# Kernel tuning notes

Measured on AMD Instinct MI355X. Metric: run time of the kernel, lower is better.

The kernel has to match this reference:

```python
import jax, jax.numpy as jnp
import numpy as np
import math

DIM_IN = 512
DIM_OUT = 512
KERNEL = 3
STYLE_DIM = 2 * 128
LIN_SCALE = 1.0 / math.sqrt(STYLE_DIM)      # EqualLinear scale (lr_mul=1)
CONV_SCALE = 1.0 / math.sqrt(DIM_IN * KERNEL ** 2)  # fan_in = dim_in * k**2 (as in source)
PAD = KERNEL // 2


def setup_inputs() -> dict:
    key = jax.random.key(0)
    ks = jax.random.split(key, 5)
    B, T = 16, 2048
    x = jax.random.normal(ks[0], (B, DIM_IN, T), dtype=jnp.float32)
    c_src = jax.random.normal(ks[1], (B, 128), dtype=jnp.float32)
    c_trg = jax.random.normal(ks[2], (B, 128), dtype=jnp.float32)
    style_w = jax.random.normal(ks[3], (DIM_IN, STYLE_DIM), dtype=jnp.float32)
    style_b = jnp.ones((DIM_IN,), dtype=jnp.float32)  # bias_init=1
    weight = jax.random.normal(ks[4], (1, DIM_OUT, DIM_IN, KERNEL), dtype=jnp.float32)
    return {"x": x, "c_src": c_src, "c_trg": c_trg,
            "style_w": style_w, "style_b": style_b, "weight": weight}


def reference(x, c_src, c_trg, style_w, style_b, weight):
    B = x.shape[0]
    # EqualLinear: style code s [B, dim_in]
    c = jnp.concatenate([c_src, c_trg], axis=-1)              # [B, 256]
    s = c @ (style_w * LIN_SCALE).T + style_b                 # [B, dim_in]
    # Modulate: w [B, dim_out, dim_in, k]
    w = CONV_SCALE * weight * s[:, None, :, None]
    # Demodulate over (dim_in, k)
    demod = jax.lax.rsqrt(jnp.sum(w * w, axis=(2, 3)) + 1e-8)  # [B, dim_out]
    w = w * demod[:, :, None, None]
    # Per-sample conv1d, padding 'same' (pad = k//2), vmapped over batch
    def conv1(xi, wi):
        # xi: [dim_in, T], wi: [dim_out, dim_in, k]
        out = jax.lax.conv_general_dilated(
            xi[None], wi, window_strides=(1,), padding=[(PAD, PAD)],
            dimension_numbers=("NCH", "OIH", "NCH"))
        return out[0]                                          # [dim_out, T]
    return jax.vmap(conv1)(x, w)                               # [B, dim_out, T]
```

## Files before the change

### kernel.cpp

```cpp
#include <hip/hip_runtime.h>
#include <cstdint>
#include <cstddef>


#define LIN_SCALE  0.0625f
#define CONV_SCALE 0.014731391f

#define B_   16
#define CIN  512
#define COUT 512
#define T_   2048
#define TP   2050

typedef __bf16 bf16x8 __attribute__((ext_vector_type(8)));
typedef float  f32x4  __attribute__((ext_vector_type(4)));
typedef unsigned short u16x8 __attribute__((ext_vector_type(8)));
typedef unsigned short u16x2 __attribute__((ext_vector_type(2)));

#define AS1 __attribute__((address_space(1)))
#define AS3 __attribute__((address_space(3)))

__device__ inline unsigned short f2bf(float f) {
  __bf16 h = (__bf16)f;
  return __builtin_bit_cast(unsigned short, h);
}

__global__ __launch_bounds__(256) void style_kernel(const float* __restrict__ c_src,
                                                    const float* __restrict__ c_trg,
                                                    const float* __restrict__ sw,
                                                    const float* __restrict__ sb,
                                                    float* __restrict__ s) {
  __shared__ float c[256];
  const int b = blockIdx.y;
  const int tid = threadIdx.x;
  c[tid] = (tid < 128) ? c_src[b * 128 + tid] : c_trg[b * 128 + tid - 128];
  __syncthreads();
  const int w = tid >> 6, lane = tid & 63;
  #pragma unroll
  for (int rr = 0; rr < 16; ++rr) {
    const int i = blockIdx.x * 64 + w * 16 + rr;
    const float* row = sw + (size_t)i * 256;
    float acc = row[lane] * c[lane] + row[lane + 64] * c[lane + 64]
              + row[lane + 128] * c[lane + 128] + row[lane + 192] * c[lane + 192];
    #pragma unroll
    for (int off = 32; off; off >>= 1) acc += __shfl_down(acc, off, 64);
    if (lane == 0) s[b * 512 + i] = acc * LIN_SCALE + sb[i];
  }
}

__global__ __launch_bounds__(256) void modw_kernel(const float* __restrict__ weight,
                                                   const float* __restrict__ s,
                                                   unsigned short* __restrict__ Wm) {
  const int o = blockIdx.x;
  const int tid = threadIdx.x;
  __shared__ float wsh[1536];
  __shared__ float svs[16 * 512];
  __shared__ float partial[16][4];
  __shared__ float demv[16];

  #pragma unroll
  for (int j = tid; j < 1536; j += 256) wsh[j] = weight[(size_t)o * 1536 + j];
  #pragma unroll
  for (int j = tid; j < 16 * 512; j += 256) svs[j] = s[j];
  __syncthreads();

  float wr[6];
  #pragma unroll
  for (int q = 0; q < 6; ++q) wr[q] = wsh[tid * 6 + q] * CONV_SCALE;

  const int lane = tid & 63, w = tid >> 6;
  float ssb[16];
  #pragma unroll
  for (int b = 0; b < 16; ++b) {
    const float s0 = svs[b * 512 + 2 * tid];
    const float s1 = svs[b * 512 + 2 * tid + 1];
    float ss = 0.f;
    #pragma unroll
    for (int q = 0; q < 3; ++q) { float v = wr[q] * s0; ss += v * v; }
    #pragma unroll
    for (int q = 3; q < 6; ++q) { float v = wr[q] * s1; ss += v * v; }
    ssb[b] = ss;
  }
  #pragma unroll
  for (int b = 0; b < 16; ++b) {
    float ss = ssb[b];
    #pragma unroll
    for (int off = 32; off; off >>= 1) ss += __shfl_down(ss, off, 64);
    if (lane == 0) partial[b][w] = ss;
  }
  __syncthreads();
  if (tid < 16)
    demv[tid] = rsqrtf(partial[tid][0] + partial[tid][1] + partial[tid][2] + partial[tid][3] + 1e-8f);
  __syncthreads();

  #pragma unroll
  for (int b = 0; b < 16; ++b) {
    const float dem = demv[b];
    const float s0 = svs[b * 512 + 2 * tid] * dem;
    const float s1 = svs[b * 512 + 2 * tid + 1] * dem;
    #pragma unroll
    for (int k = 0; k < 3; ++k) {
      u16x2 v;
      v.x = f2bf(wr[k] * s0);
      v.y = f2bf(wr[3 + k] * s1);
      *(u16x2*)&Wm[(((size_t)b * 3 + k) * 512 + o) * 512 + 2 * tid] = v;
    }
  }
}

__global__ __launch_bounds__(256) void transpose_kernel(const float* __restrict__ x,
                                                        unsigned short* __restrict__ xT) {
  __shared__ float tile[64][65];
  const int b = blockIdx.z, i0 = blockIdx.y * 64, t0 = blockIdx.x * 64;
  const int tid = threadIdx.x;

  const int lr = tid >> 4;
  const int lc = (tid & 15) * 4;
  const float* xb = x + ((size_t)b * CIN + i0) * T_ + t0;
  #pragma unroll
  for (int p = 0; p < 4; ++p) {
    const int r = p * 16 + lr;
    const float4 v = *(const float4*)(xb + (size_t)r * T_ + lc);
    tile[r][lc + 0] = v.x; tile[r][lc + 1] = v.y;
    tile[r][lc + 2] = v.z; tile[r][lc + 3] = v.w;
  }
  if (blockIdx.x == 0 && tid < 8)
    *(u16x8*)&xT[(size_t)b * TP * CIN + i0 + tid * 8] = (u16x8){0,0,0,0,0,0,0,0};
  if (blockIdx.x == gridDim.x - 1 && tid < 8)
    *(u16x8*)&xT[((size_t)b * TP + TP - 1) * CIN + i0 + tid * 8] = (u16x8){0,0,0,0,0,0,0,0};
  __syncthreads();

  const int st = tid >> 3;
  const int si = (tid & 7) * 8;
  unsigned short* xTb = xT + ((size_t)b * TP + 1 + t0) * CIN + i0;
  #pragma unroll
  for (int p = 0; p < 2; ++p) {
    const int t = p * 32 + st;
    u16x8 v;
    #pragma unroll
    for (int q = 0; q < 8; ++q) v[q] = f2bf(tile[si + q][t]);
    *(u16x8*)&xTb[(size_t)t * CIN + si] = v;
  }
}

#define BM 128
#define BN 256
#define BK 32

__global__ __launch_bounds__(256, 2) void gemm_kernel(const unsigned short* __restrict__ Wm,
                                                      const unsigned short* __restrict__ xT,
                                                      float* __restrict__ out) {
  __shared__ unsigned short lA[3 * 128 * 32];
  __shared__ unsigned short lB[258 * 32];

  const int id  = blockIdx.x;
  const int xcd = id & 7;
  const int j   = id >> 3;
  const int b   = xcd + 8 * (j >> 5);
  const int r   = j & 31;
  const int o0  = (r >> 3) * BM;
  const int t0  = (r & 7) * BN;

  const int tid  = threadIdx.x;
  const int lane = tid & 63;
  const int wm   = ((tid >> 6) & 1) * 64;
  const int wn   = (tid >> 7) * 128;
  const int rl   = lane & 15;
  const int kc   = lane >> 4;

  const unsigned short* gW = Wm + ((size_t)b * 3 * 512 + o0) * 512;
  const unsigned short* gX = xT + ((size_t)b * TP + t0) * CIN;

  f32x4 acc[4][8];
  #pragma unroll
  for (int i = 0; i < 4; ++i)
    #pragma unroll
    for (int jj = 0; jj < 8; ++jj) acc[i][jj] = (f32x4){0.f, 0.f, 0.f, 0.f};

  for (int kk = 0; kk < 16; ++kk) {
    const int i0 = kk * 32;
    __syncthreads();
    #pragma unroll
    for (int q = 0; q < 6; ++q) {
      const int ci  = q * 256 + tid;
      const int row = ci >> 2;
      const int tap = row >> 7;
      const int ar  = row & 127;
      const int gc  = ((ci & 3) ^ ((ar >> 1) & 3)) * 8;
      __builtin_amdgcn_global_load_lds(
          (const AS1 void*)(gW + (size_t)tap * 262144 + (size_t)ar * 512 + i0 + gc),
          (AS3 void*)(&lA[ci * 8]), 16, 0, 0);
    }
    #pragma unroll
    for (int q = 0; q < 4; ++q) {
      const int ci  = q * 256 + tid;
      const int row = ci >> 2;
      const int gc  = ((ci & 3) ^ ((row >> 1) & 3)) * 8;
      __builtin_amdgcn_global_load_lds(
          (const AS1 void*)(gX + (size_t)row * CIN + i0 + gc),
          (AS3 void*)(&lB[ci * 8]), 16, 0, 0);
    }
    if (tid < 8) {
      const int ci  = 1024 + tid;
      const int row = ci >> 2;
      const int gc  = ((ci & 3) ^ ((row >> 1) & 3)) * 8;
      __builtin_amdgcn_global_load_lds(
          (const AS1 void*)(gX + (size_t)row * CIN + i0 + gc),
          (AS3 void*)(&lB[ci * 8]), 16, 0, 0);
    }
    __syncthreads();

    #pragma unroll
    for (int tap = 0; tap < 3; ++tap) {
      bf16x8 af[4], bfr[8];
      #pragma unroll
      for (int mi = 0; mi < 4; ++mi) {
        const int ra = wm + mi * 16 + rl;
        af[mi] = *(const bf16x8*)&lA[((tap * 128 + ra) * 4 + (kc ^ ((ra >> 1) & 3))) * 8];
      }
      #pragma unroll
      for (int ni = 0; ni < 8; ++ni) {
        const int rb = wn + ni * 16 + rl + tap;
        bfr[ni] = *(const bf16x8*)&lB[(rb * 4 + (kc ^ ((rb >> 1) & 3))) * 8];
      }
      #pragma unroll
      for (int mi = 0; mi < 4; ++mi)
        #pragma unroll
        for (int ni = 0; ni < 8; ++ni)
          acc[mi][ni] = __builtin_amdgcn_mfma_f32_16x16x32_bf16(af[mi], bfr[ni], acc[mi][ni], 0, 0, 0);
    }
  }

  float* ob = out + ((size_t)b * COUT + o0 + wm) * T_ + t0 + wn;
  const int rrow = (lane >> 4) * 4;
  const int ccol = lane & 15;
  #pragma unroll
  for (int mi = 0; mi < 4; ++mi)
    #pragma unroll
    for (int ni = 0; ni < 8; ++ni)
      #pragma unroll
      for (int rr = 0; rr < 4; ++rr)
        ob[(size_t)(mi * 16 + rrow + rr) * T_ + ni * 16 + ccol] = acc[mi][ni][rr];
}

extern "C" void kernel_launch(void* const* d_in, const int* in_sizes, int n_in,
                              void* d_out, int out_size, void* d_ws, size_t ws_size,
                              hipStream_t stream) {
  const float* x       = (const float*)d_in[0];
  const float* c_src   = (const float*)d_in[1];
  const float* c_trg   = (const float*)d_in[2];
  const float* style_w = (const float*)d_in[3];
  const float* style_b = (const float*)d_in[4];
  const float* weight  = (const float*)d_in[5];
  float* out = (float*)d_out;

  char* ws = (char*)d_ws;
  float* s_buf          = (float*)ws;
  unsigned short* Wm    = (unsigned short*)(ws + 32768);
  unsigned short* xTbuf = (unsigned short*)(ws + 32768 + 25165824);

  style_kernel<<<dim3(8, 16), 256, 0, stream>>>(c_src, c_trg, style_w, style_b, s_buf);
  modw_kernel<<<dim3(COUT), 256, 0, stream>>>(weight, s_buf, Wm);
  transpose_kernel<<<dim3(T_ / 64, CIN / 64, B_), 256, 0, stream>>>(x, xTbuf);
  gemm_kernel<<<dim3(512), 256, 0, stream>>>(Wm, xTbuf, out);
}
```

Baseline: 187.1 us.

## Warp-specialize GEMM with a producer wave double-buffering LDS tiles

Adds a fifth wavefront to each GEMM block that issues every global-to-LDS tile load into a double buffer. The four compute waves now synchronize through LDS ready/done counters instead of block-wide barriers. The aim is to overlap memory loads with MFMA work and to take the load issue off the compute waves. In exchange, LDS use doubles and launch bounds drop to one block per CU, and spin-waiting adds overhead. It is also unclear whether the block-level fence guarantees the async global_load_lds writes have landed before the ready flag is set.

```diff
diff --git a/kernel.cpp b/kernel.cpp
--- a/kernel.cpp
+++ b/kernel.cpp
@@ -146,12 +146,16 @@
 #define BM 128
 #define BN 256
 #define BK 32
-
-__global__ __launch_bounds__(256, 2) void gemm_kernel(const unsigned short* __restrict__ Wm,
+#define LA_SZ (3 * 128 * 32)
+#define LB_SZ (258 * 32)
+
+__global__ __launch_bounds__(320, 1) void gemm_kernel(const unsigned short* __restrict__ Wm,
                                                       const unsigned short* __restrict__ xT,
                                                       float* __restrict__ out) {
-  __shared__ unsigned short lA[3 * 128 * 32];
-  __shared__ unsigned short lB[258 * 32];
+  __shared__ unsigned short lA[2 * LA_SZ];
+  __shared__ unsigned short lB[2 * LB_SZ];
+  __shared__ int ready[2];
+  __shared__ int done[2];
 
   const int id  = blockIdx.x;
   const int xcd = id & 7;
@@ -163,14 +167,55 @@
 
   const int tid  = threadIdx.x;
   const int lane = tid & 63;
-  const int wm   = ((tid >> 6) & 1) * 64;
-  const int wn   = (tid >> 7) * 128;
-  const int rl   = lane & 15;
-  const int kc   = lane >> 4;
+  const int wid  = tid >> 6;
 
   const unsigned short* gW = Wm + ((size_t)b * 3 * 512 + o0) * 512;
   const unsigned short* gX = xT + ((size_t)b * TP + t0) * CIN;
 
+  if (tid < 2) { ready[tid] = 0; done[tid] = 0; }
+  __syncthreads();
+
+  if (wid == 4) {
+    for (int kk = 0; kk < 16; ++kk) {
+      const int p  = kk & 1;
+      const int u  = kk >> 1;
+      const int i0 = kk * 32;
+      while (__hip_atomic_load(&done[p], __ATOMIC_ACQUIRE, __HIP_MEMORY_SCOPE_WORKGROUP) < 4 * u)
+        __builtin_amdgcn_s_sleep(1);
+      #pragma unroll
+      for (int q = 0; q < 24; ++q) {
+        const int ci  = q * 64 + lane;
+        const int row = ci >> 2;
+        const int tap = row >> 7;
+        const int ar  = row & 127;
+        const int gc  = ((ci & 3) ^ ((ar >> 1) & 3)) * 8;
+        __builtin_amdgcn_global_load_lds(
+            (const AS1 void*)(gW + (size_t)tap * 262144 + (size_t)ar * 512 + i0 + gc),
+            (AS3 void*)(&lA[p * LA_SZ + ci * 8]), 16, 0, 0);
+      }
+      #pragma unroll
+      for (int q = 0; q < 17; ++q) {
+        const int ci = q * 64 + lane;
+        if (ci < 1032) {
+          const int row = ci >> 2;
+          const int gc  = ((ci & 3) ^ ((row >> 1) & 3)) * 8;
+          __builtin_amdgcn_global_load_lds(
+              (const AS1 void*)(gX + (size_t)row * CIN + i0 + gc),
+              (AS3 void*)(&lB[p * LB_SZ + ci * 8]), 16, 0, 0);
+        }
+      }
+      __threadfence_block();
+      if (lane == 0)
+        __hip_atomic_fetch_add(&ready[p], 1, __ATOMIC_RELEASE, __HIP_MEMORY_SCOPE_WORKGROUP);
+    }
+    return;
+  }
+
+  const int wm = (wid & 1) * 64;
+  const int wn = (wid >> 1) * 128;
+  const int rl = lane & 15;
+  const int kc = lane >> 4;
+
   f32x4 acc[4][8];
   #pragma unroll
   for (int i = 0; i < 4; ++i)
@@ -178,37 +223,12 @@
     for (int jj = 0; jj < 8; ++jj) acc[i][jj] = (f32x4){0.f, 0.f, 0.f, 0.f};
 
   for (int kk = 0; kk < 16; ++kk) {
-    const int i0 = kk * 32;
-    __syncthreads();
-    #pragma unroll
-    for (int q = 0; q < 6; ++q) {
-      const int ci  = q * 256 + tid;
-      const int row = ci >> 2;
-      const int tap = row >> 7;
-      const int ar  = row & 127;
-      const int gc  = ((ci & 3) ^ ((ar >> 1) & 3)) * 8;
-      __builtin_amdgcn_global_load_lds(
-          (const AS1 void*)(gW + (size_t)tap * 262144 + (size_t)ar * 512 + i0 + gc),
-          (AS3 void*)(&lA[ci * 8]), 16, 0, 0);
-    }
-    #pragma unroll
-    for (int q = 0; q < 4; ++q) {
-      const int ci  = q * 256 + tid;
-      const int row = ci >> 2;
-      const int gc  = ((ci & 3) ^ ((row >> 1) & 3)) * 8;
-      __builtin_amdgcn_global_load_lds(
-          (const AS1 void*)(gX + (size_t)row * CIN + i0 + gc),
-          (AS3 void*)(&lB[ci * 8]), 16, 0, 0);
-    }
-    if (tid < 8) {
-      const int ci  = 1024 + tid;
-      const int row = ci >> 2;
-      const int gc  = ((ci & 3) ^ ((row >> 1) & 3)) * 8;
-      __builtin_amdgcn_global_load_lds(
-          (const AS1 void*)(gX + (size_t)row * CIN + i0 + gc),
-          (AS3 void*)(&lB[ci * 8]), 16, 0, 0);
-    }
-    __syncthreads();
+    const int p = kk & 1;
+    const int u = kk >> 1;
+    while (__hip_atomic_load(&ready[p], __ATOMIC_ACQUIRE, __HIP_MEMORY_SCOPE_WORKGROUP) < u + 1)
+      __builtin_amdgcn_s_sleep(1);
+    const int ca = p * LA_SZ;
+    const int cb = p * LB_SZ;
 
     #pragma unroll
     for (int tap = 0; tap < 3; ++tap) {
@@ -216,12 +236,12 @@
       #pragma unroll
       for (int mi = 0; mi < 4; ++mi) {
         const int ra = wm + mi * 16 + rl;
-        af[mi] = *(const bf16x8*)&lA[((tap * 128 + ra) * 4 + (kc ^ ((ra >> 1) & 3))) * 8];
+        af[mi] = *(const bf16x8*)&lA[ca + ((tap * 128 + ra) * 4 + (kc ^ ((ra >> 1) & 3))) * 8];
       }
       #pragma unroll
       for (int ni = 0; ni < 8; ++ni) {
         const int rb = wn + ni * 16 + rl + tap;
-        bfr[ni] = *(const bf16x8*)&lB[(rb * 4 + (kc ^ ((rb >> 1) & 3))) * 8];
+        bfr[ni] = *(const bf16x8*)&lB[cb + (rb * 4 + (kc ^ ((rb >> 1) & 3))) * 8];
       }
       #pragma unroll
       for (int mi = 0; mi < 4; ++mi)
@@ -229,6 +249,8 @@
         for (int ni = 0; ni < 8; ++ni)
           acc[mi][ni] = __builtin_amdgcn_mfma_f32_16x16x32_bf16(af[mi], bfr[ni], acc[mi][ni], 0, 0, 0);
     }
+    if (lane == 0)
+      __hip_atomic_fetch_add(&done[p], 1, __ATOMIC_RELEASE, __HIP_MEMORY_SCOPE_WORKGROUP);
   }
 
   float* ob = out + ((size_t)b * COUT + o0 + wm) * T_ + t0 + wn;
@@ -262,5 +284,5 @@
   style_kernel<<<dim3(8, 16), 256, 0, stream>>>(c_src, c_trg, style_w, style_b, s_buf);
   modw_kernel<<<dim3(COUT), 256, 0, stream>>>(weight, s_buf, Wm);
   transpose_kernel<<<dim3(T_ / 64, CIN / 64, B_), 256, 0, stream>>>(x, xTbuf);
-  gemm_kernel<<<dim3(512), 256, 0, stream>>>(Wm, xTbuf, out);
-}
+  gemm_kernel<<<dim3(512), 320, 0, stream>>>(Wm, xTbuf, out);
+}
```

Result: no change. 190.2 us (+1.6%).
